# Kernel optimization log

Measured on AMD Instinct MI355X. Metric: run time of the kernel, lower is better.

Reference implementation:

```python
import jax, jax.numpy as jnp
import numpy as np

N_NODES = 50000
N_EDGES = 800000
N_GRAPHS = 256
IN_DIM, HID = 300, 256
C1, C2, C3 = 16, 64, 256


def setup_inputs() -> dict:
    key = jax.random.key(0)
    ks = jax.random.split(key, 16)
    inp = {
        "x": jax.random.normal(ks[0], (N_NODES, IN_DIM), dtype=jnp.float32),
        "edge_index": jax.random.randint(ks[1], (2, N_EDGES), 0, N_NODES, dtype=jnp.int64),
        "batch": jnp.sort(jax.random.randint(ks[2], (N_NODES,), 0, N_GRAPHS, dtype=jnp.int64)),
    }
    def lin(k, fan_in, fan_out):
        s = 1.0 / np.sqrt(fan_in)
        kw, kb = jax.random.split(k)
        return (jax.random.uniform(kw, (fan_in, fan_out), minval=-s, maxval=s, dtype=jnp.float32),
                jax.random.uniform(kb, (fan_out,), minval=-s, maxval=s, dtype=jnp.float32))
    inp["W1"], inp["b1"] = lin(ks[3], IN_DIM, HID)
    inp["W2"], inp["b2"] = lin(ks[4], HID, HID)
    inp["W3"], inp["b3"] = lin(ks[5], HID, HID)
    inp["Wc1"], inp["bc1"] = lin(ks[6], HID, C1)
    inp["Wc2"], inp["bc2"] = lin(ks[7], HID + C1, C2)
    inp["Wc3"], inp["bc3"] = lin(ks[8], HID + C2, C3)
    return inp


def reference(x, edge_index, batch, W1, b1, W2, b2, W3, b3, Wc1, bc1, Wc2, bc2, Wc3, bc3):
    N = x.shape[0]
    loop = jnp.arange(N, dtype=edge_index.dtype)
    src = jnp.concatenate([edge_index[0], loop])   # source nodes (+ self-loops)
    dst = jnp.concatenate([edge_index[1], loop])   # target nodes (+ self-loops)
    # symmetric GCN normalization: deg^{-1/2}[src] * deg^{-1/2}[dst], deg incl self-loops
    deg = jax.ops.segment_sum(jnp.ones(src.shape, x.dtype), dst, num_segments=N)
    dinv = jnp.where(deg > 0, jax.lax.rsqrt(deg), 0.0)
    norm = dinv[src] * dinv[dst]                   # [E+N]

    def gcn_conv(h, W, b):
        h = h @ W                                  # transform first (PyG order)
        msg = h[src] * norm[:, None]               # gather + scale
        return jax.ops.segment_sum(msg, dst, num_segments=N) + b  # scatter-add

    h = jax.nn.relu(gcn_conv(x, W1, b1))           # dropout = identity (eval)
    h = jax.nn.relu(gcn_conv(h, W2, b2))
    h = gcn_conv(h, W3, b3)

    # global mean pool over graphs
    cnt = jax.ops.segment_sum(jnp.ones((N,), x.dtype), batch, num_segments=N_GRAPHS)
    pooled = jax.ops.segment_sum(h, batch, num_segments=N_GRAPHS) / jnp.maximum(cnt, 1.0)[:, None]

    l1 = pooled @ Wc1 + bc1
    p1 = jax.nn.softmax(l1, axis=1)
    l2 = jnp.concatenate([pooled, p1], axis=1) @ Wc2 + bc2
    p2 = jax.nn.softmax(l2, axis=1)
    l3 = jnp.concatenate([pooled, p2], axis=1) @ Wc3 + bc3
    return (l1, l2, l3)
```

## Files before the change

### kernel.cpp

```cpp
#include <hip/hip_runtime.h>
#include <hip/hip_bf16.h>

#define N_NODES 50000
#define N_EDGES 800000
#define N_GRAPHS 256
#define IN_DIM 300
#define HID 256
#define ROWS_PAD 50048
#define GB2 782
#define EPB 1024
#define FILLB 782

typedef __bf16 bf16x8 __attribute__((ext_vector_type(8)));
typedef short  s16x8  __attribute__((ext_vector_type(8)));
typedef short  s16x4  __attribute__((ext_vector_type(4)));
typedef float  f32x4  __attribute__((ext_vector_type(4)));
typedef float  f32x2  __attribute__((ext_vector_type(2)));
typedef int    i32x4  __attribute__((ext_vector_type(4)));

static __device__ __forceinline__ ushort f2bf(float f) {
    union { float f; uint u; } v; v.f = f;
    uint u = v.u;
    uint r = (u + 0x7fffu + ((u >> 16) & 1u)) >> 16;
    return (ushort)r;
}
static __device__ __forceinline__ float bf2f(ushort b) {
    union { uint u; float f; } v; v.u = ((uint)b) << 16;
    return v.f;
}
static __device__ __forceinline__ unsigned char f2fp8(float f) {
    int pk = __builtin_amdgcn_cvt_pk_fp8_f32(f, f, 0, 0);
    return (unsigned char)(pk & 0xff);
}


__global__ __launch_bounds__(256) void pre_k(const float* __restrict__ W1,
                                             const float* __restrict__ W2,
                                             const float* __restrict__ W3,
                                             ushort* __restrict__ Wt1,
                                             ushort* __restrict__ Wt2,
                                             ushort* __restrict__ Wt3,
                                             const int* __restrict__ dst,
                                             int* __restrict__ cnt) {
    int b = blockIdx.x;
    int n = threadIdx.x;
    if (b < 320) {
        int k = b;
        Wt1[(size_t)n * 320 + k] = (k < IN_DIM) ? f2bf(W1[(size_t)k * 256 + n]) : (ushort)0;
    } else if (b < 576) {
        int k = b - 320;
        Wt2[(size_t)n * 256 + k] = f2bf(W2[(size_t)k * 256 + n]);
    } else if (b < 832) {
        int k = b - 576;
        Wt3[(size_t)n * 256 + k] = f2bf(W3[(size_t)k * 256 + n]);
    } else {
        int e0 = (b - 832) * EPB + n * 4;
        if (e0 + 4 <= N_EDGES) {
            i32x4 d = *(const i32x4*)(dst + e0);
            atomicAdd(&cnt[d[0]], 1);
            atomicAdd(&cnt[d[1]], 1);
            atomicAdd(&cnt[d[2]], 1);
            atomicAdd(&cnt[d[3]], 1);
        } else {
            for (int j = 0; j < 4; ++j)
                if (e0 + j < N_EDGES) atomicAdd(&cnt[dst[e0 + j]], 1);
        }
    }
}


__global__ void scan1(const int* __restrict__ cnt, int* __restrict__ rp,
                      int* __restrict__ bsums, float* __restrict__ dinv, int n) {
    __shared__ int s[256];
    int i = blockIdx.x * 256 + threadIdx.x;
    int v = (i < n) ? cnt[i] : 0;
    if (i < n) dinv[i] = rsqrtf((float)(v + 1));
    s[threadIdx.x] = v;
    __syncthreads();
    for (int off = 1; off < 256; off <<= 1) {
        int t = (threadIdx.x >= off) ? s[threadIdx.x - off] : 0;
        __syncthreads();
        s[threadIdx.x] += t;
        __syncthreads();
    }
    if (i < n) rp[i] = s[threadIdx.x] - v;
    if (threadIdx.x == 255) bsums[blockIdx.x] = s[255];
}

__global__ void scan2(int* __restrict__ bsums, int nb) {
    __shared__ int s[256];
    int v = (threadIdx.x < nb) ? bsums[threadIdx.x] : 0;
    s[threadIdx.x] = v;
    __syncthreads();
    for (int off = 1; off < 256; off <<= 1) {
        int t = (threadIdx.x >= off) ? s[threadIdx.x - off] : 0;
        __syncthreads();
        s[threadIdx.x] += t;
        __syncthreads();
    }
    if (threadIdx.x < nb) bsums[threadIdx.x] = s[threadIdx.x] - v;
}

__global__ void scan3(int* __restrict__ rp, int* __restrict__ cursor,
                      const int* __restrict__ bsums, int n) {
    int i = blockIdx.x * 256 + threadIdx.x;
    if (i < n) {
        int v = rp[i] + bsums[blockIdx.x];
        rp[i] = v;
        cursor[i] = v;
    }
}


template <int KP, int KACT, bool AF32>
static __device__ __forceinline__ void gemm_body(int bx, const void* __restrict__ Ap,
                                                 const ushort* __restrict__ Bt,
                                                 unsigned char* __restrict__ C, int M,
                                                 ushort* As, ushort* Bs) {
    int t = threadIdx.x;
    int wave = t >> 6, lane = t & 63, quad = lane >> 4, l16 = lane & 15;
    int wm = wave >> 1, wn = wave & 1;
    int r0 = (bx >> 1) * 128;
    int n0 = (bx & 1) * 128;
    int srow = t & 127;
    int shalf = t >> 7;

    f32x4 acc[4][4] = {};

    for (int kc = 0; kc < KP; kc += 64) {
#pragma unroll
        for (int i = 0; i < 4; ++i) {
            int ks = 2 * i + shalf;
            *(s16x8*)(Bs + ks * 1024 + srow * 8) =
                *(const s16x8*)(Bt + (size_t)(n0 + srow) * KP + kc + ks * 8);
        }
#pragma unroll
        for (int i = 0; i < 4; ++i) {
            int ks = 2 * i + shalf;
            int kg = kc + ks * 8;
            if constexpr (AF32) {
                const float* Af = (const float*)Ap;
                int rg = r0 + srow; if (rg >= M) rg = M - 1;
                ushort tmp[8];
                if (kg + 8 <= KACT) {
                    f32x4 f0 = *(const f32x4*)(Af + (size_t)rg * KACT + kg);
                    f32x4 f1 = *(const f32x4*)(Af + (size_t)rg * KACT + kg + 4);
#pragma unroll
                    for (int j = 0; j < 4; ++j) { tmp[j] = f2bf(f0[j]); tmp[4 + j] = f2bf(f1[j]); }
                } else if (kg < KACT) {
                    f32x4 f0 = *(const f32x4*)(Af + (size_t)rg * KACT + kg);
#pragma unroll
                    for (int j = 0; j < 4; ++j) { tmp[j] = f2bf(f0[j]); tmp[4 + j] = 0; }
                } else {
#pragma unroll
                    for (int j = 0; j < 8; ++j) tmp[j] = 0;
                }
                *(s16x8*)(As + ks * 1024 + srow * 8) = *(const s16x8*)tmp;
            } else {
                const ushort* A = (const ushort*)Ap;
                *(s16x8*)(As + ks * 1024 + srow * 8) =
                    *(const s16x8*)(A + (size_t)(r0 + srow) * KP + kg);
            }
        }
        __syncthreads();

#pragma unroll
        for (int ks2 = 0; ks2 < 2; ++ks2) {
            bf16x8 a[4], b[4];
#pragma unroll
            for (int ct = 0; ct < 4; ++ct)
                b[ct] = __builtin_bit_cast(bf16x8,
                    *(const s16x8*)(Bs + (ks2 * 4 + quad) * 1024 + (wn * 64 + ct * 16 + l16) * 8));
#pragma unroll
            for (int rt = 0; rt < 4; ++rt)
                a[rt] = __builtin_bit_cast(bf16x8,
                    *(const s16x8*)(As + (ks2 * 4 + quad) * 1024 + (wm * 64 + rt * 16 + l16) * 8));
#pragma unroll
            for (int rt = 0; rt < 4; ++rt)
#pragma unroll
                for (int ct = 0; ct < 4; ++ct)
                    acc[rt][ct] = __builtin_amdgcn_mfma_f32_16x16x32_bf16(a[rt], b[ct], acc[rt][ct], 0, 0, 0);
        }
        __syncthreads();
    }

#pragma unroll
    for (int rt = 0; rt < 4; ++rt) {
        int rowb = r0 + wm * 64 + rt * 16 + quad * 4;
#pragma unroll
        for (int ct = 0; ct < 4; ++ct) {
            int col = n0 + wn * 64 + ct * 16 + l16;
#pragma unroll
            for (int i = 0; i < 4; ++i)
                C[(size_t)(rowb + i) * 256 + col] = f2fp8(acc[rt][ct][i]);
        }
    }
}

template <int KP, int KACT, bool AF32>
__global__ __launch_bounds__(256, 4) void gemm_k(const void* __restrict__ Ap,
                                                 const ushort* __restrict__ Bt,
                                                 unsigned char* __restrict__ C, int M) {
    __shared__ __align__(16) ushort As[8 * 128 * 8];
    __shared__ __align__(16) ushort Bs[8 * 128 * 8];
    gemm_body<KP, KACT, AF32>(blockIdx.x, Ap, Bt, C, M, As, Bs);
}

__global__ __launch_bounds__(256, 3) void gemm1_fill(const float* __restrict__ x,
                                                     const ushort* __restrict__ Wt1,
                                                     unsigned char* __restrict__ C, int M,
                                                     const int* __restrict__ src,
                                                     const int* __restrict__ dst,
                                                     int* __restrict__ cursor,
                                                     int* __restrict__ col) {
    __shared__ __align__(16) ushort As[8 * 128 * 8];
    __shared__ __align__(16) ushort Bs[8 * 128 * 8];
    int b = blockIdx.x;
    if (b < GB2) {
        gemm_body<320, IN_DIM, true>(b, x, Wt1, C, M, As, Bs);
    } else {
        int e0 = (b - GB2) * EPB + threadIdx.x * 4;
        if (e0 + 4 <= N_EDGES) {
            i32x4 d = *(const i32x4*)(dst + e0);
            i32x4 s = *(const i32x4*)(src + e0);
            int p0 = atomicAdd(&cursor[d[0]], 1);
            int p1 = atomicAdd(&cursor[d[1]], 1);
            int p2 = atomicAdd(&cursor[d[2]], 1);
            int p3 = atomicAdd(&cursor[d[3]], 1);
            col[p0] = s[0]; col[p1] = s[1]; col[p2] = s[2]; col[p3] = s[3];
        } else {
            for (int j = 0; j < 4; ++j) {
                int e = e0 + j;
                if (e < N_EDGES) {
                    int p = atomicAdd(&cursor[dst[e]], 1);
                    col[p] = src[e];
                }
            }
        }
    }
}


__global__ __launch_bounds__(256) void aggregate_fp8(const unsigned char* __restrict__ z,
                                                     ushort* __restrict__ out,
                                                     const int* __restrict__ rp,
                                                     const int* __restrict__ cnt,
                                                     const int* __restrict__ col,
                                                     const float* __restrict__ dinv,
                                                     const float* __restrict__ bias, int relu) {
    const uint* zu = (const uint*)z;
    int t = threadIdx.x;
    int wave = __builtin_amdgcn_readfirstlane(t >> 6);
    int lane = t & 63;
    int n = blockIdx.x * 4 + wave;
    int start = rp[n];
    int c = cnt[n];
    float dv = dinv[n];

    float a0 = 0.f, a1 = 0.f, a2 = 0.f, a3 = 0.f;

    int j = 0;
    for (; j + 4 <= c; j += 4) {
        int r0 = col[start + j], r1 = col[start + j + 1];
        int r2 = col[start + j + 2], r3 = col[start + j + 3];
        float w0 = dinv[r0], w1 = dinv[r1], w2 = dinv[r2], w3 = dinv[r3];
        uint v0 = zu[(size_t)r0 * 64 + lane];
        uint v1 = zu[(size_t)r1 * 64 + lane];
        uint v2 = zu[(size_t)r2 * 64 + lane];
        uint v3 = zu[(size_t)r3 * 64 + lane];
        f32x2 p, q;
        p = __builtin_amdgcn_cvt_pk_f32_fp8(v0, 0); q = __builtin_amdgcn_cvt_pk_f32_fp8(v0, 1);
        a0 += w0 * p[0]; a1 += w0 * p[1]; a2 += w0 * q[0]; a3 += w0 * q[1];
        p = __builtin_amdgcn_cvt_pk_f32_fp8(v1, 0); q = __builtin_amdgcn_cvt_pk_f32_fp8(v1, 1);
        a0 += w1 * p[0]; a1 += w1 * p[1]; a2 += w1 * q[0]; a3 += w1 * q[1];
        p = __builtin_amdgcn_cvt_pk_f32_fp8(v2, 0); q = __builtin_amdgcn_cvt_pk_f32_fp8(v2, 1);
        a0 += w2 * p[0]; a1 += w2 * p[1]; a2 += w2 * q[0]; a3 += w2 * q[1];
        p = __builtin_amdgcn_cvt_pk_f32_fp8(v3, 0); q = __builtin_amdgcn_cvt_pk_f32_fp8(v3, 1);
        a0 += w3 * p[0]; a1 += w3 * p[1]; a2 += w3 * q[0]; a3 += w3 * q[1];
    }
    for (; j < c; ++j) {
        int r = col[start + j];
        float w = dinv[r];
        uint v = zu[(size_t)r * 64 + lane];
        f32x2 p = __builtin_amdgcn_cvt_pk_f32_fp8(v, 0);
        f32x2 q = __builtin_amdgcn_cvt_pk_f32_fp8(v, 1);
        a0 += w * p[0]; a1 += w * p[1]; a2 += w * q[0]; a3 += w * q[1];
    }

    uint vs = zu[(size_t)n * 64 + lane];
    f32x2 sp = __builtin_amdgcn_cvt_pk_f32_fp8(vs, 0);
    f32x2 sq = __builtin_amdgcn_cvt_pk_f32_fp8(vs, 1);
    float sv[4] = {sp[0], sp[1], sq[0], sq[1]};
    f32x4 bv = *(const f32x4*)(bias + lane * 4);
    ushort o[4];
#pragma unroll
    for (int i = 0; i < 4; ++i) {
        float acc = (i == 0 ? a0 : i == 1 ? a1 : i == 2 ? a2 : a3);
        float r = dv * (acc + dv * sv[i]) + bv[i];
        if (relu) r = fmaxf(r, 0.f);
        o[i] = f2bf(r);
    }
    *(s16x4*)(out + (size_t)n * HID + (size_t)lane * 4) = *(const s16x4*)o;
}


__global__ __launch_bounds__(256) void pool_sum(const ushort* __restrict__ h,
                                                const int* __restrict__ batch,
                                                float* __restrict__ psum, int n) {
    int f = threadIdx.x;
    int r0 = blockIdx.x * 64;
    int rend = min(r0 + 64, n);
    if (r0 >= n) return;
    int g = batch[r0];
    float acc = 0.f;
    for (int r = r0; r < rend; ++r) {
        int gr = batch[r];
        if (gr != g) {
            atomicAdd(&psum[g * HID + f], acc);
            acc = 0.f;
            g = gr;
        }
        acc += bf2f(h[(size_t)r * HID + f]);
    }
    atomicAdd(&psum[g * HID + f], acc);
}


__global__ __launch_bounds__(256) void head_k(const float* __restrict__ psum,
                                              const int* __restrict__ batch, int n,
                                              const float* __restrict__ Wc1, const float* __restrict__ bc1,
                                              const float* __restrict__ Wc2, const float* __restrict__ bc2,
                                              const float* __restrict__ Wc3, const float* __restrict__ bc3,
                                              float* __restrict__ out) {
    int g = blockIdx.x;
    int t = threadIdx.x;
    __shared__ float pr[256];
    __shared__ float l1s[16], p1s[16];
    __shared__ float l2s[64], p2s[64];
    int lo = 0, hi = n;
    while (lo < hi) { int mid = (lo + hi) >> 1; if (batch[mid] < g) lo = mid + 1; else hi = mid; }
    int start = lo;
    lo = start; hi = n;
    while (lo < hi) { int mid = (lo + hi) >> 1; if (batch[mid] < g + 1) lo = mid + 1; else hi = mid; }
    int c = lo - start;
    float inv_c = 1.f / (float)max(c, 1);
    pr[t] = psum[g * 256 + t] * inv_c;
    __syncthreads();
    if (t < 16) {
        float a = bc1[t];
        for (int k = 0; k < 256; ++k) a += pr[k] * Wc1[k * 16 + t];
        l1s[t] = a;
        out[g * 16 + t] = a;
    }
    __syncthreads();
    if (t == 0) {
        float m = -1e30f;
        for (int j = 0; j < 16; ++j) m = fmaxf(m, l1s[j]);
        float s = 0.f;
        for (int j = 0; j < 16; ++j) { float e = expf(l1s[j] - m); p1s[j] = e; s += e; }
        float inv = 1.f / s;
        for (int j = 0; j < 16; ++j) p1s[j] *= inv;
    }
    __syncthreads();
    if (t < 64) {
        float a = bc2[t];
        for (int k = 0; k < 256; ++k) a += pr[k] * Wc2[k * 64 + t];
        for (int k = 0; k < 16; ++k) a += p1s[k] * Wc2[(256 + k) * 64 + t];
        l2s[t] = a;
        out[4096 + g * 64 + t] = a;
    }
    __syncthreads();
    if (t == 0) {
        float m = -1e30f;
        for (int j = 0; j < 64; ++j) m = fmaxf(m, l2s[j]);
        float s = 0.f;
        for (int j = 0; j < 64; ++j) { float e = expf(l2s[j] - m); p2s[j] = e; s += e; }
        float inv = 1.f / s;
        for (int j = 0; j < 64; ++j) p2s[j] *= inv;
    }
    __syncthreads();
    {
        float a = bc3[t];
        for (int k = 0; k < 256; ++k) a += pr[k] * Wc3[k * 256 + t];
        for (int k = 0; k < 64; ++k) a += p2s[k] * Wc3[(256 + k) * 256 + t];
        out[4096 + 16384 + g * 256 + t] = a;
    }
}


extern "C" void kernel_launch(void* const* d_in, const int* in_sizes, int n_in,
                              void* d_out, int out_size, void* d_ws, size_t ws_size,
                              hipStream_t stream) {
    const float* x    = (const float*)d_in[0];
    const int*   ei   = (const int*)d_in[1];
    const int*   batch= (const int*)d_in[2];
    const float* W1 = (const float*)d_in[3];  const float* b1 = (const float*)d_in[4];
    const float* W2 = (const float*)d_in[5];  const float* b2 = (const float*)d_in[6];
    const float* W3 = (const float*)d_in[7];  const float* b3 = (const float*)d_in[8];
    const float* Wc1= (const float*)d_in[9];  const float* bc1= (const float*)d_in[10];
    const float* Wc2= (const float*)d_in[11]; const float* bc2= (const float*)d_in[12];
    const float* Wc3= (const float*)d_in[13]; const float* bc3= (const float*)d_in[14];
    float* out = (float*)d_out;

    const int N = N_NODES, E = N_EDGES, G = N_GRAPHS;

    char* ws = (char*)d_ws;
    size_t off = 0;
    auto alloc = [&](size_t bytes) -> void* {
        void* p = ws + off;
        off = (off + bytes + 255) & ~(size_t)255;
        return p;
    };
    unsigned char* z = (unsigned char*)alloc((size_t)ROWS_PAD * HID);
    ushort* hb   = (ushort*)alloc((size_t)ROWS_PAD * HID * 2);
    ushort* Wt1  = (ushort*)alloc((size_t)256 * 320 * 2);
    ushort* Wt2  = (ushort*)alloc((size_t)256 * 256 * 2);
    ushort* Wt3  = (ushort*)alloc((size_t)256 * 256 * 2);
    int*   cnt    = (int*)alloc((size_t)N * 4);
    int*   rp     = (int*)alloc((size_t)N * 4);
    int*   cursor = (int*)alloc((size_t)N * 4);
    float* dinv   = (float*)alloc((size_t)N * 4);
    int*   col    = (int*)alloc((size_t)E * 4);
    float* psum   = (float*)alloc((size_t)G * HID * 4);
    int*   bsums  = (int*)alloc(256 * 4);
    (void)ws_size;

    const int* src = ei;
    const int* dst = ei + E;

    hipMemsetAsync(cnt, 0, (size_t)N * 4, stream);
    hipMemsetAsync(psum, 0, (size_t)G * HID * 4, stream);

    pre_k<<<832 + FILLB, 256, 0, stream>>>(W1, W2, W3, Wt1, Wt2, Wt3, dst, cnt);

    const int NB = (N + 255) / 256;
    scan1<<<NB, 256, 0, stream>>>(cnt, rp, bsums, dinv, N);
    scan2<<<1, 256, 0, stream>>>(bsums, NB);
    scan3<<<NB, 256, 0, stream>>>(rp, cursor, bsums, N);

    gemm1_fill<<<GB2 + FILLB, 256, 0, stream>>>(x, Wt1, z, N, src, dst, cursor, col);

    aggregate_fp8<<<N / 4, 256, 0, stream>>>(z, hb, rp, cnt, col, dinv, b1, 1);
    gemm_k<256, 256, false><<<GB2, 256, 0, stream>>>(hb, Wt2, z, N);
    aggregate_fp8<<<N / 4, 256, 0, stream>>>(z, hb, rp, cnt, col, dinv, b2, 1);
    gemm_k<256, 256, false><<<GB2, 256, 0, stream>>>(hb, Wt3, z, N);
    aggregate_fp8<<<N / 4, 256, 0, stream>>>(z, hb, rp, cnt, col, dinv, b3, 0);

    pool_sum<<<ROWS_PAD / 64, 256, 0, stream>>>(hb, batch, psum, N);
    head_k<<<G, 256, 0, stream>>>(psum, batch, N, Wc1, bc1, Wc2, bc2, Wc3, bc3, out);
}
```

Before: 432.7 us.

## Fuse mean-pool sum into final aggregation and reorder edge-fill blocks first

The last GCN aggregation now reduces its four node rows per block in shared memory and atomically adds them into the per-graph pooled sums, removing the separate pool_sum kernel and the bf16 write and read of the final hidden layer. Pooling also now sums the fp32 values rather than bf16-rounded ones. Separately, the edge-counting and CSR-fill blocks are placed at the start of the pre_k and gemm1_fill grids, ahead of the weight-transpose and GEMM blocks, so the atomic-heavy work is scheduled first. The cost is more atomics on psum (up to four per feature per block) plus a block-wide barrier in the fused aggregation.

```diff
diff --git a/kernel.cpp b/kernel.cpp
--- a/kernel.cpp
+++ b/kernel.cpp
@@ -44,17 +44,8 @@
                                              int* __restrict__ cnt) {
     int b = blockIdx.x;
     int n = threadIdx.x;
-    if (b < 320) {
-        int k = b;
-        Wt1[(size_t)n * 320 + k] = (k < IN_DIM) ? f2bf(W1[(size_t)k * 256 + n]) : (ushort)0;
-    } else if (b < 576) {
-        int k = b - 320;
-        Wt2[(size_t)n * 256 + k] = f2bf(W2[(size_t)k * 256 + n]);
-    } else if (b < 832) {
-        int k = b - 576;
-        Wt3[(size_t)n * 256 + k] = f2bf(W3[(size_t)k * 256 + n]);
-    } else {
-        int e0 = (b - 832) * EPB + n * 4;
+    if (b < FILLB) {
+        int e0 = b * EPB + n * 4;
         if (e0 + 4 <= N_EDGES) {
             i32x4 d = *(const i32x4*)(dst + e0);
             atomicAdd(&cnt[d[0]], 1);
@@ -65,6 +56,15 @@
             for (int j = 0; j < 4; ++j)
                 if (e0 + j < N_EDGES) atomicAdd(&cnt[dst[e0 + j]], 1);
         }
+    } else if (b < FILLB + 320) {
+        int k = b - FILLB;
+        Wt1[(size_t)n * 320 + k] = (k < IN_DIM) ? f2bf(W1[(size_t)k * 256 + n]) : (ushort)0;
+    } else if (b < FILLB + 576) {
+        int k = b - (FILLB + 320);
+        Wt2[(size_t)n * 256 + k] = f2bf(W2[(size_t)k * 256 + n]);
+    } else {
+        int k = b - (FILLB + 576);
+        Wt3[(size_t)n * 256 + k] = f2bf(W3[(size_t)k * 256 + n]);
     }
 }
 
@@ -216,10 +216,8 @@
     __shared__ __align__(16) ushort As[8 * 128 * 8];
     __shared__ __align__(16) ushort Bs[8 * 128 * 8];
     int b = blockIdx.x;
-    if (b < GB2) {
-        gemm_body<320, IN_DIM, true>(b, x, Wt1, C, M, As, Bs);
-    } else {
-        int e0 = (b - GB2) * EPB + threadIdx.x * 4;
+    if (b < FILLB) {
+        int e0 = b * EPB + threadIdx.x * 4;
         if (e0 + 4 <= N_EDGES) {
             i32x4 d = *(const i32x4*)(dst + e0);
             i32x4 s = *(const i32x4*)(src + e0);
@@ -237,17 +235,22 @@
                 }
             }
         }
-    }
-}
-
-
+    } else {
+        gemm_body<320, IN_DIM, true>(b - FILLB, x, Wt1, C, M, As, Bs);
+    }
+}
+
+
+template <bool TO_PSUM>
 __global__ __launch_bounds__(256) void aggregate_fp8(const unsigned char* __restrict__ z,
                                                      ushort* __restrict__ out,
                                                      const int* __restrict__ rp,
                                                      const int* __restrict__ cnt,
                                                      const int* __restrict__ col,
                                                      const float* __restrict__ dinv,
-                                                     const float* __restrict__ bias, int relu) {
+                                                     const float* __restrict__ bias, int relu,
+                                                     const int* __restrict__ batch,
+                                                     float* __restrict__ psum) {
     const uint* zu = (const uint*)z;
     int t = threadIdx.x;
     int wave = __builtin_amdgcn_readfirstlane(t >> 6);
@@ -292,37 +295,36 @@
     f32x2 sq = __builtin_amdgcn_cvt_pk_f32_fp8(vs, 1);
     float sv[4] = {sp[0], sp[1], sq[0], sq[1]};
     f32x4 bv = *(const f32x4*)(bias + lane * 4);
-    ushort o[4];
-#pragma unroll
-    for (int i = 0; i < 4; ++i) {
-        float acc = (i == 0 ? a0 : i == 1 ? a1 : i == 2 ? a2 : a3);
-        float r = dv * (acc + dv * sv[i]) + bv[i];
-        if (relu) r = fmaxf(r, 0.f);
-        o[i] = f2bf(r);
-    }
-    *(s16x4*)(out + (size_t)n * HID + (size_t)lane * 4) = *(const s16x4*)o;
-}
-
-
-__global__ __launch_bounds__(256) void pool_sum(const ushort* __restrict__ h,
-                                                const int* __restrict__ batch,
-                                                float* __restrict__ psum, int n) {
-    int f = threadIdx.x;
-    int r0 = blockIdx.x * 64;
-    int rend = min(r0 + 64, n);
-    if (r0 >= n) return;
-    int g = batch[r0];
-    float acc = 0.f;
-    for (int r = r0; r < rend; ++r) {
-        int gr = batch[r];
-        if (gr != g) {
-            atomicAdd(&psum[g * HID + f], acc);
-            acc = 0.f;
-            g = gr;
-        }
-        acc += bf2f(h[(size_t)r * HID + f]);
-    }
-    atomicAdd(&psum[g * HID + f], acc);
+
+    if constexpr (!TO_PSUM) {
+        ushort o[4];
+#pragma unroll
+        for (int i = 0; i < 4; ++i) {
+            float acc = (i == 0 ? a0 : i == 1 ? a1 : i == 2 ? a2 : a3);
+            float r = dv * (acc + dv * sv[i]) + bv[i];
+            if (relu) r = fmaxf(r, 0.f);
+            o[i] = f2bf(r);
+        }
+        *(s16x4*)(out + (size_t)n * HID + (size_t)lane * 4) = *(const s16x4*)o;
+    } else {
+        __shared__ float sred[4][256];
+        __shared__ int sg[4];
+#pragma unroll
+        for (int i = 0; i < 4; ++i) {
+            float acc = (i == 0 ? a0 : i == 1 ? a1 : i == 2 ? a2 : a3);
+            sred[wave][lane * 4 + i] = dv * (acc + dv * sv[i]) + bv[i];
+        }
+        if (lane == 0) sg[wave] = batch[n];
+        __syncthreads();
+        float acc = sred[0][t];
+        int g = sg[0];
+        for (int w = 1; w < 4; ++w) {
+            int gw = sg[w];
+            if (gw == g) acc += sred[w][t];
+            else { atomicAdd(&psum[g * HID + t], acc); g = gw; acc = sred[w][t]; }
+        }
+        atomicAdd(&psum[g * HID + t], acc);
+    }
 }
 
 
@@ -431,21 +433,20 @@
     hipMemsetAsync(cnt, 0, (size_t)N * 4, stream);
     hipMemsetAsync(psum, 0, (size_t)G * HID * 4, stream);
 
-    pre_k<<<832 + FILLB, 256, 0, stream>>>(W1, W2, W3, Wt1, Wt2, Wt3, dst, cnt);
+    pre_k<<<FILLB + 832, 256, 0, stream>>>(W1, W2, W3, Wt1, Wt2, Wt3, dst, cnt);
 
     const int NB = (N + 255) / 256;
     scan1<<<NB, 256, 0, stream>>>(cnt, rp, bsums, dinv, N);
     scan2<<<1, 256, 0, stream>>>(bsums, NB);
     scan3<<<NB, 256, 0, stream>>>(rp, cursor, bsums, N);
 
-    gemm1_fill<<<GB2 + FILLB, 256, 0, stream>>>(x, Wt1, z, N, src, dst, cursor, col);
-
-    aggregate_fp8<<<N / 4, 256, 0, stream>>>(z, hb, rp, cnt, col, dinv, b1, 1);
+    gemm1_fill<<<FILLB + GB2, 256, 0, stream>>>(x, Wt1, z, N, src, dst, cursor, col);
+
+    aggregate_fp8<false><<<N / 4, 256, 0, stream>>>(z, hb, rp, cnt, col, dinv, b1, 1, batch, psum);
     gemm_k<256, 256, false><<<GB2, 256, 0, stream>>>(hb, Wt2, z, N);
-    aggregate_fp8<<<N / 4, 256, 0, stream>>>(z, hb, rp, cnt, col, dinv, b2, 1);
+    aggregate_fp8<false><<<N / 4, 256, 0, stream>>>(z, hb, rp, cnt, col, dinv, b2, 1, batch, psum);
     gemm_k<256, 256, false><<<GB2, 256, 0, stream>>>(hb, Wt3, z, N);
-    aggregate_fp8<<<N / 4, 256, 0, stream>>>(z, hb, rp, cnt, col, dinv, b3, 0);
-
-    pool_sum<<<ROWS_PAD / 64, 256, 0, stream>>>(hb, batch, psum, N);
+    aggregate_fp8<true><<<N / 4, 256, 0, stream>>>(z, hb, rp, cnt, col, dinv, b3, 0, batch, psum);
+
     head_k<<<G, 256, 0, stream>>>(psum, batch, N, Wc1, bc1, Wc2, bc2, Wc3, bc3, out);
 }
```

New measurement: 444.6 us. 2.8% more time.
